# Kernel tuning notes

Hardware: AMD Instinct MI355X
Metric: run time of the kernel (lower is better)

The kernel has to match this reference:

```python
import jax, jax.numpy as jnp
import numpy as np

N_NODES = 100000
N_FEAT = 128
N_CLASSES = 40
N_EDGES = 1600000
K_HOPS = 2


def setup_inputs() -> dict:
    key = jax.random.key(0)
    k1, k2, k3 = jax.random.split(key, 3)
    x = jax.random.normal(k1, (N_NODES, N_FEAT), dtype=jnp.float32)
    edge_index = jax.random.randint(k2, (2, N_EDGES), 0, N_NODES, dtype=jnp.int32)
    W = jax.random.normal(k3, (N_FEAT, N_CLASSES), dtype=jnp.float32) * 0.05
    b = jnp.zeros((N_CLASSES,), dtype=jnp.float32)
    return {"x": x, "W": W, "b": b, "edge_index": edge_index, "K": K_HOPS}


def reference(x, W, b, edge_index, K):
    N = x.shape[0]
    src, dst = edge_index[0], edge_index[1]
    # Add self-loops (GCN normalization, as in PyG gcn_norm)
    loop = jnp.arange(N, dtype=src.dtype)
    src = jnp.concatenate([src, loop])
    dst = jnp.concatenate([dst, loop])
    # Symmetric normalization: deg^{-1/2} A_hat deg^{-1/2}
    deg = jnp.zeros((N,), dtype=x.dtype).at[dst].add(jnp.ones_like(dst, dtype=x.dtype))
    deg_inv_sqrt = jnp.where(deg > 0, jax.lax.rsqrt(jnp.maximum(deg, 1.0)), 0.0)
    norm = deg_inv_sqrt[src] * deg_inv_sqrt[dst]  # [E+N]
    for _ in range(K):
        msgs = norm[:, None] * x[src]  # gather [E+N, F]
        x = jax.ops.segment_sum(msgs, dst, num_segments=N)
    logits = x @ W + b  # [N, C]
    return jax.nn.log_softmax(logits, axis=1)
```

## Files before the change

kernel.cpp:

```cpp
#include <hip/hip_runtime.h>
#include <math.h>


#define FDIM 128
#define CDIM 40
#define BKT_SHIFT 8
#define NB   512
#define NBLK 512
#define NPB  25
#define ZSTR 8

typedef __attribute__((ext_vector_type(4))) float floatx4;
typedef __attribute__((ext_vector_type(8))) short bshort8;

__device__ __forceinline__ unsigned int bf16rn(float f) {
    unsigned int u = __float_as_uint(f);
    return (u + 0x7fffu + ((u >> 16) & 1u)) >> 16;
}
__device__ __forceinline__ unsigned int pack2(float lo, float hi) {
    unsigned int a = bf16rn(lo);
    unsigned int b = __float_as_uint(hi);
    b = (b + 0x7fffu + ((b >> 16) & 1u)) & 0xffff0000u;
    return a | b;
}
__device__ __forceinline__ void addu4(uint4 u, float* a) {
    a[0] += __uint_as_float(u.x << 16);
    a[1] += __uint_as_float(u.x & 0xffff0000u);
    a[2] += __uint_as_float(u.y << 16);
    a[3] += __uint_as_float(u.y & 0xffff0000u);
    a[4] += __uint_as_float(u.z << 16);
    a[5] += __uint_as_float(u.z & 0xffff0000u);
    a[6] += __uint_as_float(u.w << 16);
    a[7] += __uint_as_float(u.w & 0xffff0000u);
}

__global__ void hist_k(const int* __restrict__ dst, int* __restrict__ G,
                       int E, int EB, const float* __restrict__ W,
                       uint4* __restrict__ WF) {
    int t = threadIdx.x;
    if (blockIdx.x == NBLK) {
        for (int s = t; s < 768; s += 256) {
            int l = s & 63;
            int g = s >> 6;
            int nt = g >> 2;
            int ch = g & 3;
            int c = nt * 16 + (l & 15);
            int kb = ch * 32 + ((l >> 4) << 3);
            unsigned int hw[4], lw[4];
            #pragma unroll
            for (int jw = 0; jw < 4; ++jw) {
                unsigned int hs[2], ls[2];
                #pragma unroll
                for (int e = 0; e < 2; ++e) {
                    int j = jw * 2 + e;
                    float w = (c < CDIM) ? W[(kb + j) * CDIM + c] : 0.f;
                    unsigned int u = __float_as_uint(w);
                    float wh = __uint_as_float(u & 0xffff0000u);
                    float wr = w - wh;
                    hs[e] = u >> 16;
                    ls[e] = __float_as_uint(wr) >> 16;
                }
                hw[jw] = hs[0] | (hs[1] << 16);
                lw[jw] = ls[0] | (ls[1] << 16);
            }
            WF[g * 64 + l] = make_uint4(hw[0], hw[1], hw[2], hw[3]);
            WF[768 + g * 64 + l] = make_uint4(lw[0], lw[1], lw[2], lw[3]);
        }
        return;
    }
    __shared__ int h[NB];
    for (int i = t; i < NB; i += 256) h[i] = 0;
    __syncthreads();
    int s = blockIdx.x * EB;
    int e = min(s + EB, E);
    for (int i = s + t; i < e; i += 256)
        atomicAdd(&h[dst[i] >> BKT_SHIFT], 1);
    __syncthreads();
    for (int i = t; i < NB; i += 256) G[blockIdx.x * NB + i] = h[i];
}

__global__ void colscan_k(int* __restrict__ G, int* __restrict__ T) {
    __shared__ int lds[256];
    int j = blockIdx.x;
    int t = threadIdx.x;
    int v0 = G[(2 * t) * NB + j];
    int v1 = G[(2 * t + 1) * NB + j];
    int s = v0 + v1;
    lds[t] = s;
    __syncthreads();
    for (int off = 1; off < 256; off <<= 1) {
        int a = (t >= off) ? lds[t - off] : 0;
        __syncthreads();
        lds[t] += a;
        __syncthreads();
    }
    int excl = lds[t] - s;
    G[(2 * t) * NB + j] = excl;
    G[(2 * t + 1) * NB + j] = excl + v0;
    if (t == 255) T[j] = lds[255];
}

__global__ void bscan_k(const int* __restrict__ T, int* __restrict__ bs) {
    __shared__ int lds[256];
    int t = threadIdx.x;
    int v0 = T[2 * t];
    int v1 = T[2 * t + 1];
    int s = v0 + v1;
    lds[t] = s;
    __syncthreads();
    for (int off = 1; off < 256; off <<= 1) {
        int a = (t >= off) ? lds[t - off] : 0;
        __syncthreads();
        lds[t] += a;
        __syncthreads();
    }
    int excl = lds[t] - s;
    bs[2 * t] = excl;
    bs[2 * t + 1] = excl + v0;
    if (t == 255) bs[NB] = lds[255];
}

__global__ void part_k(const int* __restrict__ src, const int* __restrict__ dst,
                       const int* __restrict__ G, const int* __restrict__ bs,
                       unsigned int* __restrict__ tmp, int E, int EB) {
    __shared__ int offs[NB];
    __shared__ int cur[NB];
    int t = threadIdx.x;
    for (int i = t; i < NB; i += 256) {
        offs[i] = bs[i] + G[blockIdx.x * NB + i];
        cur[i] = 0;
    }
    __syncthreads();
    int s = blockIdx.x * EB;
    int e = min(s + EB, E);
    for (int i = s + t; i < e; i += 256) {
        int d = dst[i];
        int j = d >> BKT_SHIFT;
        int r = atomicAdd(&cur[j], 1);
        tmp[offs[j] + r] = (unsigned int)src[i] | ((unsigned int)(d & 255) << 24);
    }
}

__global__ void csr_k(const unsigned int* __restrict__ tmp, const int* __restrict__ bs,
                      int* __restrict__ rowptr, float* __restrict__ dinv,
                      float* __restrict__ dsq, int* __restrict__ col, int N, int E) {
    __shared__ int cnt[256];
    __shared__ int ptr[256];
    int j = blockIdx.x;
    int t = threadIdx.x;
    int base = j << BKT_SHIFT;
    int s = bs[j];
    int e = bs[j + 1];
    cnt[t] = 0;
    __syncthreads();
    for (int i = s + t; i < e; i += 256)
        atomicAdd(&cnt[tmp[i] >> 24], 1);
    __syncthreads();
    int v = cnt[t];
    ptr[t] = v;
    __syncthreads();
    for (int off = 1; off < 256; off <<= 1) {
        int a = (t >= off) ? ptr[t - off] : 0;
        __syncthreads();
        ptr[t] += a;
        __syncthreads();
    }
    int excl = ptr[t] - v;
    int node = base + t;
    if (node < N) {
        rowptr[node] = s + excl;
        float d = (float)(v + 1);
        dinv[node] = rsqrtf(d);
        dsq[node] = sqrtf(d);
    }
    if (j == 0 && t == 0) rowptr[N] = E;
    cnt[t] = excl;
    __syncthreads();
    for (int i = s + t; i < e; i += 256) {
        unsigned int p = tmp[i];
        int loc = p >> 24;
        int r = atomicAdd(&cnt[loc], 1);
        col[s + r] = (int)(p & 0xFFFFFF);
    }
}

__device__ __forceinline__ void split8(const float* p, bshort8& hi, bshort8& lo) {
    float4 a = *(const float4*)p;
    float4 b = *(const float4*)(p + 4);
    float f[8] = {a.x, a.y, a.z, a.w, b.x, b.y, b.z, b.w};
    #pragma unroll
    for (int j = 0; j < 8; ++j) {
        unsigned int u = __float_as_uint(f[j]);
        float r = f[j] - __uint_as_float(u & 0xffff0000u);
        hi[j] = (short)(u >> 16);
        lo[j] = (short)(__float_as_uint(r) >> 16);
    }
}

#define EPS 52

__global__ __launch_bounds__(256) void gemm_k(const float* __restrict__ x,
                                              const uint4* __restrict__ WF,
                                              const float* __restrict__ dinv,
                                              uint4* __restrict__ Zbf, int n) {
    __shared__ float ep[64 * EPS];
    int t = threadIdx.x;
    int wid = t >> 6;
    int l = t & 63;
    int lr = l & 15;
    int lg = l >> 4;
    int base64 = blockIdx.x * 64;
    int mbase = base64 + wid * 16;
    int node_a = mbase + lr;
    bool arow_ok = node_a < n;
    const bshort8* WFv = (const bshort8*)WF;

    floatx4 acc0 = {0.f, 0.f, 0.f, 0.f};
    floatx4 acc1 = {0.f, 0.f, 0.f, 0.f};
    floatx4 acc2 = {0.f, 0.f, 0.f, 0.f};

    #pragma unroll
    for (int ch = 0; ch < 4; ++ch) {
        bshort8 ah, al;
        if (arow_ok) {
            split8(x + (size_t)node_a * FDIM + ch * 32 + lg * 8, ah, al);
        } else {
            #pragma unroll
            for (int j = 0; j < 8; ++j) { ah[j] = 0; al[j] = 0; }
        }
        bshort8 bh0 = WFv[(0 * 4 + ch) * 64 + l];
        bshort8 bl0 = WFv[768 + (0 * 4 + ch) * 64 + l];
        bshort8 bh1 = WFv[(1 * 4 + ch) * 64 + l];
        bshort8 bl1 = WFv[768 + (1 * 4 + ch) * 64 + l];
        bshort8 bh2 = WFv[(2 * 4 + ch) * 64 + l];
        bshort8 bl2 = WFv[768 + (2 * 4 + ch) * 64 + l];
        acc0 = __builtin_amdgcn_mfma_f32_16x16x32_bf16(ah, bh0, acc0, 0, 0, 0);
        acc0 = __builtin_amdgcn_mfma_f32_16x16x32_bf16(al, bh0, acc0, 0, 0, 0);
        acc0 = __builtin_amdgcn_mfma_f32_16x16x32_bf16(ah, bl0, acc0, 0, 0, 0);
        acc1 = __builtin_amdgcn_mfma_f32_16x16x32_bf16(ah, bh1, acc1, 0, 0, 0);
        acc1 = __builtin_amdgcn_mfma_f32_16x16x32_bf16(al, bh1, acc1, 0, 0, 0);
        acc1 = __builtin_amdgcn_mfma_f32_16x16x32_bf16(ah, bl1, acc1, 0, 0, 0);
        acc2 = __builtin_amdgcn_mfma_f32_16x16x32_bf16(ah, bh2, acc2, 0, 0, 0);
        acc2 = __builtin_amdgcn_mfma_f32_16x16x32_bf16(al, bh2, acc2, 0, 0, 0);
        acc2 = __builtin_amdgcn_mfma_f32_16x16x32_bf16(ah, bl2, acc2, 0, 0, 0);
    }

    int nlb = wid * 16 + 4 * lg;
    #pragma unroll
    for (int r = 0; r < 4; ++r) {
        int nd = mbase + 4 * lg + r;
        float di = (nd < n) ? dinv[nd] : 0.f;
        ep[(nlb + r) * EPS + 0 * 16 + lr] = acc0[r] * di;
        ep[(nlb + r) * EPS + 1 * 16 + lr] = acc1[r] * di;
        ep[(nlb + r) * EPS + 2 * 16 + lr] = acc2[r] * di;
    }
    __syncthreads();
    for (int i = t; i < 320; i += 256) {
        int nl2 = i / 5;
        int cg = i - nl2 * 5;
        int node = base64 + nl2;
        if (node < n) {
            const float* p = &ep[nl2 * EPS + cg * 8];
            float4 v0 = *(const float4*)p;
            float4 v1 = *(const float4*)(p + 4);
            uint4 o;
            o.x = pack2(v0.x, v0.y);
            o.y = pack2(v0.z, v0.w);
            o.z = pack2(v1.x, v1.y);
            o.w = pack2(v1.z, v1.w);
            Zbf[(size_t)node * ZSTR + cg] = o;
        }
    }
}

template <bool FINAL>
__global__ __launch_bounds__(256) void prop_k(const int* __restrict__ rowptr,
                                              const int* __restrict__ col,
                                              const float* __restrict__ dinv,
                                              const float* __restrict__ dsq,
                                              const float* __restrict__ bias,
                                              const uint4* __restrict__ Zin,
                                              uint4* __restrict__ Zout_bf,
                                              float* __restrict__ out_f32, int n) {
    __shared__ float bsm[CDIM];
    __shared__ float red[256];
    __shared__ float pr[NPB * 5 * 8];
    int t = threadIdx.x;
    if (FINAL && t < CDIM) bsm[t] = bias[t];
    int g = t / 10;
    int r = t - g * 10;
    int team = r / 5;
    int c8 = r - team * 5;
    int node = blockIdx.x * NPB + g;
    bool active = (g < NPB) && (node < n);
    float acc[8];
    #pragma unroll
    for (int c = 0; c < 8; ++c) acc[c] = 0.f;
    float w = 0.f;
    if (active) {
        float di = dinv[node];
        w = di * di;
        if (team == 0) addu4(Zin[(size_t)node * ZSTR + c8], acc);
        int end = rowptr[node + 1];
        int e = rowptr[node] + team * 4;
        for (; e + 3 < end; e += 8) {
            int s0 = col[e], s1 = col[e + 1], s2 = col[e + 2], s3 = col[e + 3];
            uint4 a0 = Zin[(size_t)s0 * ZSTR + c8];
            uint4 a1 = Zin[(size_t)s1 * ZSTR + c8];
            uint4 a2 = Zin[(size_t)s2 * ZSTR + c8];
            uint4 a3 = Zin[(size_t)s3 * ZSTR + c8];
            addu4(a0, acc); addu4(a1, acc); addu4(a2, acc); addu4(a3, acc);
        }
        for (; e < end; ++e)
            addu4(Zin[(size_t)col[e] * ZSTR + c8], acc);
    }

    if (active && team == 1) {
        float* p = &pr[(g * 5 + c8) * 8];
        #pragma unroll
        for (int j = 0; j < 8; ++j) p[j] = acc[j];
    }
    __syncthreads();
    if (active && team == 0) {
        const float* p = &pr[(g * 5 + c8) * 8];
        #pragma unroll
        for (int j = 0; j < 8; ++j) acc[j] += p[j];
    }

    if (!FINAL) {
        if (active && team == 0) {
            uint4 o;
            o.x = pack2(acc[0] * w, acc[1] * w);
            o.y = pack2(acc[2] * w, acc[3] * w);
            o.z = pack2(acc[4] * w, acc[5] * w);
            o.w = pack2(acc[6] * w, acc[7] * w);
            Zout_bf[(size_t)node * ZSTR + c8] = o;
        }
        return;
    }

    float v[8];
    float m8 = -INFINITY;
    if (active && team == 0) {
        float ws_ = w * dsq[node];
        #pragma unroll
        for (int j = 0; j < 8; ++j) {
            v[j] = acc[j] * ws_ + bsm[c8 * 8 + j];
            m8 = fmaxf(m8, v[j]);
        }
    }
    red[t] = m8;
    __syncthreads();
    float m = m8;
    if (active && team == 0) {
        int rb = g * 10;
        m = fmaxf(fmaxf(fmaxf(red[rb], red[rb + 1]), fmaxf(red[rb + 2], red[rb + 3])),
                  red[rb + 4]);
    }
    float s8 = 0.f;
    if (active && team == 0) {
        #pragma unroll
        for (int j = 0; j < 8; ++j) s8 += expf(v[j] - m);
    }
    __syncthreads();
    red[t] = s8;
    __syncthreads();
    if (active && team == 0) {
        int rb = g * 10;
        float s = (red[rb] + red[rb + 1]) + (red[rb + 2] + red[rb + 3]) + red[rb + 4];
        float ls = m + logf(s);
        float* p = out_f32 + (size_t)node * CDIM + c8 * 8;
        *(float4*)p = make_float4(v[0] - ls, v[1] - ls, v[2] - ls, v[3] - ls);
        *(float4*)(p + 4) = make_float4(v[4] - ls, v[5] - ls, v[6] - ls, v[7] - ls);
    }
}

extern "C" void kernel_launch(void* const* d_in, const int* in_sizes, int n_in,
                              void* d_out, int out_size, void* d_ws, size_t ws_size,
                              hipStream_t stream) {
    const float* x = (const float*)d_in[0];
    const float* W = (const float*)d_in[1];
    const float* b = (const float*)d_in[2];
    const int* ei = (const int*)d_in[3];

    int C = in_sizes[2];
    int F = in_sizes[1] / C;
    int N = in_sizes[0] / F;
    int E = in_sizes[3] / 2;
    const int* src = ei;
    const int* dst = ei + E;

    char* ws = (char*)d_ws;
    size_t goff = 0;
    int* G = (int*)(ws + goff);                       goff += (size_t)NBLK * NB * 4;
    int* T = (int*)(ws + goff);                       goff += (size_t)NB * 4;
    int* bs = (int*)(ws + goff);                      goff += (size_t)(NB + 1) * 4 + 12;
    goff = (goff + 15) & ~(size_t)15;
    unsigned int* tmp = (unsigned int*)(ws + goff);   goff += (size_t)E * 4;
    size_t z0bytes = (size_t)N * ZSTR * 16;
    size_t unionEnd = (z0bytes > goff) ? z0bytes : goff;
    unionEnd = (unionEnd + 15) & ~(size_t)15;
    uint4* Z0bf = (uint4*)ws;
    size_t off = unionEnd;
    int* rowptr = (int*)(ws + off); off += ((size_t)(N + 1) * 4 + 15) & ~(size_t)15;
    float* dinv = (float*)(ws + off); off += ((size_t)N * 4 + 15) & ~(size_t)15;
    float* dsq = (float*)(ws + off); off += ((size_t)N * 4 + 15) & ~(size_t)15;
    int* col = (int*)(ws + off); off += ((size_t)E * 4 + 15) & ~(size_t)15;
    uint4* Zb = (uint4*)(ws + off); off += (z0bytes + 15) & ~(size_t)15;
    uint4* WF = (uint4*)(ws + off); off += (size_t)2 * 768 * 16;

    int EB = (E + NBLK - 1) / NBLK;
    int NBr = (N + 255) >> BKT_SHIFT;

    hist_k<<<NBLK + 1, 256, 0, stream>>>(dst, G, E, EB, W, WF);
    colscan_k<<<NB, 256, 0, stream>>>(G, T);
    bscan_k<<<1, 256, 0, stream>>>(T, bs);
    part_k<<<NBLK, 256, 0, stream>>>(src, dst, G, bs, tmp, E, EB);
    csr_k<<<NBr, 256, 0, stream>>>(tmp, bs, rowptr, dinv, dsq, col, N, E);

    gemm_k<<<(N + 63) / 64, 256, 0, stream>>>(x, WF, dinv, Z0bf, N);

    int pgrid = (N + NPB - 1) / NPB;
    prop_k<false><<<pgrid, 256, 0, stream>>>(rowptr, col, dinv, dsq, b,
                                             Z0bf, Zb, nullptr, N);
    prop_k<true><<<pgrid, 256, 0, stream>>>(rowptr, col, dinv, dsq, b,
                                            Zb, nullptr, (float*)d_out, N);
}
```

Baseline: 216.4 us.

## Fold bucket scan into consumer kernels and widen gather batches in propagation

```diff
diff --git a/kernel.cpp b/kernel.cpp
--- a/kernel.cpp
+++ b/kernel.cpp
@@ -100,9 +100,8 @@
     if (t == 255) T[j] = lds[255];
 }
 
-__global__ void bscan_k(const int* __restrict__ T, int* __restrict__ bs) {
-    __shared__ int lds[256];
-    int t = threadIdx.x;
+__device__ __forceinline__ void scanT(const int* __restrict__ T, int* bsl,
+                                      int* lds, int t) {
     int v0 = T[2 * t];
     int v1 = T[2 * t + 1];
     int s = v0 + v1;
@@ -115,19 +114,23 @@
         __syncthreads();
     }
     int excl = lds[t] - s;
-    bs[2 * t] = excl;
-    bs[2 * t + 1] = excl + v0;
-    if (t == 255) bs[NB] = lds[255];
+    bsl[2 * t] = excl;
+    bsl[2 * t + 1] = excl + v0;
+    if (t == 255) bsl[NB] = lds[255];
+    __syncthreads();
 }
 
 __global__ void part_k(const int* __restrict__ src, const int* __restrict__ dst,
-                       const int* __restrict__ G, const int* __restrict__ bs,
+                       const int* __restrict__ G, const int* __restrict__ T,
                        unsigned int* __restrict__ tmp, int E, int EB) {
+    __shared__ int bsl[NB + 1];
+    __shared__ int lds[256];
     __shared__ int offs[NB];
     __shared__ int cur[NB];
     int t = threadIdx.x;
+    scanT(T, bsl, lds, t);
     for (int i = t; i < NB; i += 256) {
-        offs[i] = bs[i] + G[blockIdx.x * NB + i];
+        offs[i] = bsl[i] + G[blockIdx.x * NB + i];
         cur[i] = 0;
     }
     __syncthreads();
@@ -141,16 +144,19 @@
     }
 }
 
-__global__ void csr_k(const unsigned int* __restrict__ tmp, const int* __restrict__ bs,
+__global__ void csr_k(const unsigned int* __restrict__ tmp, const int* __restrict__ T,
                       int* __restrict__ rowptr, float* __restrict__ dinv,
                       float* __restrict__ dsq, int* __restrict__ col, int N, int E) {
+    __shared__ int bsl[NB + 1];
+    __shared__ int lds[256];
     __shared__ int cnt[256];
     __shared__ int ptr[256];
     int j = blockIdx.x;
     int t = threadIdx.x;
+    scanT(T, bsl, lds, t);
     int base = j << BKT_SHIFT;
-    int s = bs[j];
-    int e = bs[j + 1];
+    int s = bsl[j];
+    int e = bsl[j + 1];
     cnt[t] = 0;
     __syncthreads();
     for (int i = s + t; i < e; i += 256)
@@ -302,17 +308,23 @@
         w = di * di;
         if (team == 0) addu4(Zin[(size_t)node * ZSTR + c8], acc);
         int end = rowptr[node + 1];
-        int e = rowptr[node] + team * 4;
-        for (; e + 3 < end; e += 8) {
-            int s0 = col[e], s1 = col[e + 1], s2 = col[e + 2], s3 = col[e + 3];
-            uint4 a0 = Zin[(size_t)s0 * ZSTR + c8];
-            uint4 a1 = Zin[(size_t)s1 * ZSTR + c8];
-            uint4 a2 = Zin[(size_t)s2 * ZSTR + c8];
-            uint4 a3 = Zin[(size_t)s3 * ZSTR + c8];
-            addu4(a0, acc); addu4(a1, acc); addu4(a2, acc); addu4(a3, acc);
-        }
-        for (; e < end; ++e)
-            addu4(Zin[(size_t)col[e] * ZSTR + c8], acc);
+        int end1 = end - 1;
+        int e0 = rowptr[node] + team * 8;
+        for (int base = e0; base < end; base += 16) {
+            int sv[8];
+            #pragma unroll
+            for (int k = 0; k < 8; ++k)
+                sv[k] = col[min(base + k, end1)];
+            uint4 av[8];
+            #pragma unroll
+            for (int k = 0; k < 8; ++k)
+                av[k] = Zin[(size_t)sv[k] * ZSTR + c8];
+            #pragma unroll
+            for (int k = 0; k < 8; ++k) {
+                if (base + k >= end) av[k] = make_uint4(0u, 0u, 0u, 0u);
+                addu4(av[k], acc);
+            }
+        }
     }
 
     if (active && team == 1) {
@@ -394,7 +406,6 @@
     size_t goff = 0;
     int* G = (int*)(ws + goff);                       goff += (size_t)NBLK * NB * 4;
     int* T = (int*)(ws + goff);                       goff += (size_t)NB * 4;
-    int* bs = (int*)(ws + goff);                      goff += (size_t)(NB + 1) * 4 + 12;
     goff = (goff + 15) & ~(size_t)15;
     unsigned int* tmp = (unsigned int*)(ws + goff);   goff += (size_t)E * 4;
     size_t z0bytes = (size_t)N * ZSTR * 16;
@@ -409,14 +420,14 @@
     uint4* Zb = (uint4*)(ws + off); off += (z0bytes + 15) & ~(size_t)15;
     uint4* WF = (uint4*)(ws + off); off += (size_t)2 * 768 * 16;
 
+
     int EB = (E + NBLK - 1) / NBLK;
     int NBr = (N + 255) >> BKT_SHIFT;
 
     hist_k<<<NBLK + 1, 256, 0, stream>>>(dst, G, E, EB, W, WF);
     colscan_k<<<NB, 256, 0, stream>>>(G, T);
-    bscan_k<<<1, 256, 0, stream>>>(T, bs);
-    part_k<<<NBLK, 256, 0, stream>>>(src, dst, G, bs, tmp, E, EB);
-    csr_k<<<NBr, 256, 0, stream>>>(tmp, bs, rowptr, dinv, dsq, col, N, E);
+    part_k<<<NBLK, 256, 0, stream>>>(src, dst, G, T, tmp, E, EB);
+    csr_k<<<NBr, 256, 0, stream>>>(tmp, T, rowptr, dinv, dsq, col, N, E);
 
     gemm_k<<<(N + 63) / 64, 256, 0, stream>>>(x, WF, dinv, Z0bf, N);
 
```

Result: no change. 212.4 us (-1.9%).
